# Performance work log

Hardware: AMD Instinct MI355X
Metric: run time of the kernel (lower is better)

## Reference

```python
import jax, jax.numpy as jnp
import numpy as np

N_EMBD = 1024
N_HEAD = 16
HEAD_DIM = N_EMBD // N_HEAD


def setup_inputs() -> dict:
    key = jax.random.key(0)
    ks = jax.random.split(key, 9)
    B, S = 4, 2048
    s = 1.0 / np.sqrt(N_EMBD)
    return {
        "x": jax.random.normal(ks[0], (B, S, N_EMBD), dtype=jnp.float32),
        "attention_mask": jnp.ones((B, S), dtype=jnp.int32),
        "Wq": jax.random.normal(ks[1], (N_EMBD, N_EMBD), jnp.float32) * s,
        "bq": jnp.zeros((N_EMBD,), jnp.float32),
        "Wk": jax.random.normal(ks[2], (N_EMBD, N_EMBD), jnp.float32) * s,
        "bk": jnp.zeros((N_EMBD,), jnp.float32),
        "Wv": jax.random.normal(ks[3], (N_EMBD, N_EMBD), jnp.float32) * s,
        "bv": jnp.zeros((N_EMBD,), jnp.float32),
        "Wo": jax.random.normal(ks[4], (N_EMBD, N_EMBD), jnp.float32) * s,
        "bo": jnp.zeros((N_EMBD,), jnp.float32),
    }


def _split_heads(t):  # [B,S,E] -> [B,H,S,D]
    B, S, _ = t.shape
    return t.reshape(B, S, N_HEAD, HEAD_DIM).transpose(0, 2, 1, 3)


def reference(x, attention_mask, Wq, bq, Wk, bk, Wv, bv, Wo, bo):
    B, S, E = x.shape
    q = _split_heads(x @ Wq.T + bq)
    k = _split_heads(x @ Wk.T + bk)
    v = _split_heads(x @ Wv.T + bv)
    # scores: [B,H,S,S]
    scores = jnp.einsum('bhqd,bhkd->bhqk', q, k) / np.sqrt(HEAD_DIM).astype(np.float32)
    # additive mask: 0 where mask==1, -inf where mask==0, broadcast over heads/query
    mask = jnp.where(attention_mask[:, None, None, :] == 0, -jnp.inf, 0.0).astype(scores.dtype)
    scores = scores + mask
    probs = jax.nn.softmax(scores, axis=-1)  # dropout p=0 -> identity
    ctx = jnp.einsum('bhqk,bhkd->bhqd', probs, v)
    out = ctx.transpose(0, 2, 1, 3).reshape(B, S, E)
    return out @ Wo.T + bo
```

## Files before the change

### kernel.cpp

```cpp
#include <hip/hip_runtime.h>

typedef __bf16 bf16;
typedef __attribute__((ext_vector_type(2))) bf16 bf16x2;
typedef __attribute__((ext_vector_type(4))) bf16 bf16x4;
typedef __attribute__((ext_vector_type(8))) bf16 bf16x8;
typedef __attribute__((ext_vector_type(4))) float f32x4;
typedef __attribute__((ext_vector_type(16))) float f32x16;
typedef __attribute__((ext_vector_type(4))) int i32x4;
typedef __attribute__((ext_vector_type(2))) int i32x2;

#define MFMA_BF16(a, b, c) __builtin_amdgcn_mfma_f32_16x16x32_bf16((a), (b), (c), 0, 0, 0)
#define MFMA32(a, b, c)    __builtin_amdgcn_mfma_f32_32x32x16_bf16((a), (b), (c), 0, 0, 0)

constexpr int S_LEN = 2048;
constexpr int EMB   = 1024;
constexpr int NHEAD = 16;
constexpr int HDIM  = 64;
constexpr int BATCH = 4;
constexpr int NTOK  = BATCH * S_LEN;

__device__ __forceinline__ void gload_lds16(const bf16* g, bf16* l) {
    __builtin_amdgcn_global_load_lds(
        (const __attribute__((address_space(1))) void*)g,
        (__attribute__((address_space(3))) void*)l, 16, 0, 0);
}

__device__ __forceinline__ int pkbf(float a, float b) {
    bf16x2 t; t[0] = (bf16)a; t[1] = (bf16)b;
    return __builtin_bit_cast(int, t);
}

#if __has_builtin(__builtin_amdgcn_permlane32_swap)
__device__ __forceinline__ i32x2 permswap(int a, int b) {
    return __builtin_amdgcn_permlane32_swap(a, b, false, false);
}
#else
__device__ __forceinline__ i32x2 permswap(int a, int b) {
    int as = __shfl_xor(a, 32);
    int bs = __shfl_xor(b, 32);
    int hx_ = (threadIdx.x >> 5) & 1;
    i32x2 r;
    r[0] = hx_ ? bs : a;
    r[1] = hx_ ? b : as;
    return r;
}
#endif

__global__ __launch_bounds__(256)
void cvt_f32_bf16(const float* __restrict__ src, bf16* __restrict__ dst, int n4) {
    int i = blockIdx.x * 256 + threadIdx.x;
    if (i < n4) {
        f32x4 v = ((const f32x4*)src)[i];
        bf16x4 o;
        o[0] = (bf16)v[0]; o[1] = (bf16)v[1]; o[2] = (bf16)v[2]; o[3] = (bf16)v[3];
        ((bf16x4*)dst)[i] = o;
    }
}

__global__ __launch_bounds__(256)
void cvt_w4(const float* __restrict__ s0, const float* __restrict__ s1,
            const float* __restrict__ s2, const float* __restrict__ s3,
            bf16* __restrict__ dst) {
    const int a = blockIdx.y;
    const float* s = a == 0 ? s0 : (a == 1 ? s1 : (a == 2 ? s2 : s3));
    int i = blockIdx.x * 256 + threadIdx.x;
    f32x4 v = ((const f32x4*)s)[i];
    bf16x4 o;
    o[0] = (bf16)v[0]; o[1] = (bf16)v[1]; o[2] = (bf16)v[2]; o[3] = (bf16)v[3];
    ((bf16x4*)(dst + (size_t)a * EMB * EMB))[i] = o;
}

__global__ __launch_bounds__(512)
void gemm256(const bf16* __restrict__ A,
             const bf16* __restrict__ W0, const bf16* __restrict__ W1, const bf16* __restrict__ W2,
             const float* __restrict__ b0, const float* __restrict__ b1, const float* __restrict__ b2,
             void* __restrict__ d0, void* __restrict__ d1, void* __restrict__ d2,
             int fused, float q_scale)
{
    __shared__ bf16 lds_a[2][2][128 * 32];
    __shared__ bf16 lds_b[2][2][256 * 32];

    const int fb  = blockIdx.x;
    const int xcd = fb & 7;
    const int loc = fb >> 3;
    const int xi  = xcd * 8 + (loc & 7);
    const int y   = loc >> 3;

    int seg, mode, n0;
    if (fused) { seg = y >> 2; n0 = (y & 3) * 256; mode = (seg == 2) ? 1 : 0; }
    else       { seg = 0;      n0 = y * 256;        mode = 2; }
    const bf16*  W    = seg == 0 ? W0 : (seg == 1 ? W1 : W2);
    const float* bias = seg == 0 ? b0 : (seg == 1 ? b1 : b2);
    void*        C    = seg == 0 ? d0 : (seg == 1 ? d1 : d2);
    const float  osc  = (fused && seg == 0) ? q_scale : 1.0f;

    const int tid  = threadIdx.x;
    const int lane = tid & 63;
    const int w    = tid >> 6;
    const int wr   = w >> 2;
    const int wc   = w & 3;
    const int quad = lane >> 4;
    const int l16  = lane & 15;
    const int m0   = xi * 128;

#define STAGE_A(BUF, H, T) {                                                        \
    int m_ = tid >> 2, s_ = tid & 3;                                                \
    gload_lds16(A + (size_t)(m0 + m_) * EMB + (T) * 64 + (H) * 32                   \
                  + ((s_ ^ ((m_ >> 1) & 3)) << 3),                                  \
                &lds_a[BUF][H][tid * 8]);                                           \
}
#define STAGE_B(BUF, H, T) {                                                        \
    _Pragma("unroll") for (int c_ = 0; c_ < 2; ++c_) {                              \
        int idx_ = c_ * 512 + tid;                                                  \
        int n_ = idx_ >> 2, s_ = idx_ & 3;                                          \
        gload_lds16(W + (size_t)(n0 + n_) * EMB + (T) * 64 + (H) * 32               \
                      + ((s_ ^ ((n_ >> 1) & 3)) << 3),                              \
                    &lds_b[BUF][H][idx_ * 8]);                                      \
    } }

#define READ_A(DST, BUF, H, G) {                                                    \
    _Pragma("unroll") for (int i_ = 0; i_ < 2; ++i_) {                              \
        int m_ = wr * 64 + (G) * 32 + i_ * 16 + l16;                                \
        DST[i_] = *(const bf16x8*)&lds_a[BUF][H][m_ * 32 + ((quad ^ ((m_ >> 1) & 3)) << 3)]; \
    } }
#define READ_B(DST, BUF, H) {                                                       \
    _Pragma("unroll") for (int j_ = 0; j_ < 4; ++j_) {                              \
        int n_ = wc * 64 + j_ * 16 + l16;                                           \
        DST[j_] = *(const bf16x8*)&lds_b[BUF][H][n_ * 32 + ((quad ^ ((n_ >> 1) & 3)) << 3)]; \
    } }

#define MFMA_PH(AF, BF, G) {                                                        \
    __builtin_amdgcn_s_setprio(1);                                                  \
    _Pragma("unroll") for (int i_ = 0; i_ < 2; ++i_)                                \
        _Pragma("unroll") for (int j_ = 0; j_ < 4; ++j_)                            \
            acc[(G) * 2 + i_][j_] = MFMA_BF16(AF[i_], BF[j_], acc[(G) * 2 + i_][j_]); \
    __builtin_amdgcn_s_setprio(0);                                                  \
}

    f32x4 acc[4][4] = {};

    STAGE_A(0, 0, 0) STAGE_B(0, 0, 0) STAGE_A(0, 1, 0) STAGE_B(0, 1, 0)
    asm volatile("s_waitcnt vmcnt(3)" ::: "memory");
    __builtin_amdgcn_s_barrier();
    __builtin_amdgcn_sched_barrier(0);

    for (int t = 0; t < 16; ++t) {
        const int cur  = t & 1;
        const int nxt  = cur ^ 1;
        const bool more = (t + 1 < 16);
        bf16x8 afr[2], bfr[4];

        READ_B(bfr, cur, 0)
        READ_A(afr, cur, 0, 0)
        if (more) STAGE_A(nxt, 0, t + 1)
        MFMA_PH(afr, bfr, 0)

        READ_A(afr, cur, 0, 1)
        if (more) STAGE_B(nxt, 0, t + 1)
        MFMA_PH(afr, bfr, 1)
        if (more) asm volatile("s_waitcnt vmcnt(3)" ::: "memory");
        else      asm volatile("s_waitcnt vmcnt(0)" ::: "memory");
        __builtin_amdgcn_s_barrier();
        __builtin_amdgcn_sched_barrier(0);

        READ_B(bfr, cur, 1)
        READ_A(afr, cur, 1, 0)
        if (more) STAGE_A(nxt, 1, t + 1)
        MFMA_PH(afr, bfr, 0)

        READ_A(afr, cur, 1, 1)
        if (more) STAGE_B(nxt, 1, t + 1)
        MFMA_PH(afr, bfr, 1)
        if (more) {
            asm volatile("s_waitcnt vmcnt(3)" ::: "memory");
            __builtin_amdgcn_s_barrier();
            __builtin_amdgcn_sched_barrier(0);
        }
    }

#undef STAGE_A
#undef STAGE_B
#undef READ_A
#undef READ_B
#undef MFMA_PH

    #pragma unroll
    for (int ii = 0; ii < 4; ++ii) {
        #pragma unroll
        for (int j = 0; j < 4; ++j) {
            int col = n0 + wc * 64 + j * 16 + l16;
            float bv = bias[col];
            int row0 = m0 + wr * 64 + ii * 16 + quad * 4;
            if (mode == 1) {
                int bb = row0 >> 11, s0 = row0 & 2047;
                int hh = col >> 6,   d  = col & 63;
                bf16x4 pk;
                #pragma unroll
                for (int r = 0; r < 4; ++r) pk[r] = (bf16)(acc[ii][j][r] + bv);
                *(bf16x4*)((bf16*)C + (size_t)((bb * NHEAD + hh) * HDIM + d) * S_LEN + s0) = pk;
            } else if (mode == 0) {
                #pragma unroll
                for (int r = 0; r < 4; ++r)
                    ((bf16*)C)[(size_t)(row0 + r) * EMB + col] = (bf16)((acc[ii][j][r] + bv) * osc);
            } else {
                #pragma unroll
                for (int r = 0; r < 4; ++r)
                    ((float*)C)[(size_t)(row0 + r) * EMB + col] = acc[ii][j][r] + bv;
            }
        }
    }
}

__global__ __launch_bounds__(512)
void flash_attn(const bf16* __restrict__ qg, const bf16* __restrict__ kg,
                const bf16* __restrict__ vtg, const int* __restrict__ maskg,
                bf16* __restrict__ ctx)
{
    __shared__ bf16  klds[2][64 * 64];
    __shared__ bf16  vlds[2][64 * 64];
    __shared__ bf16  bias_lds[2048];
    __shared__ float stat_lds[8][32];

    const int fb  = blockIdx.x;
    const int xcd = fb & 7;
    const int rr  = fb >> 3;
    const int qi  = rr & 7;
    const int gg  = rr >> 3;
    const int g   = gg * 8 + xcd;
    const int h   = g & 15;
    const int b   = g >> 4;
    const int q0  = qi * 256;

    const int tid  = threadIdx.x;
    const int lane = tid & 63;
    const int w    = tid >> 6;
    const int l32  = lane & 31;
    const int hx   = lane >> 5;

    const int srow  = tid >> 3;
    const int sslot = (tid & 7) ^ (srow & 7);

    int ok;
    {
        int i = tid * 4;
        i32x4 mv = *(const i32x4*)(maskg + b * S_LEN + i);
        bf16x4 bb;
        ok = 1;
        #pragma unroll
        for (int r = 0; r < 4; ++r) {
            ok &= (mv[r] != 0);
            bb[r] = mv[r] ? (bf16)0.f : (bf16)(-3.0e38f);
        }
        *(bf16x4*)&bias_lds[i] = bb;
    }
    const int allvalid = __syncthreads_and(ok);

    bf16x8 qf[4];
    {
        const bf16* qrow = qg + (size_t)(b * S_LEN + q0 + w * 32 + l32) * EMB + h * HDIM + hx * 8;
        qf[0] = *(const bf16x8*)(qrow);
        qf[1] = *(const bf16x8*)(qrow + 16);
        qf[2] = *(const bf16x8*)(qrow + 32);
        qf[3] = *(const bf16x8*)(qrow + 48);
    }

    const bf16* kgb = kg  + (size_t)b * S_LEN * EMB + h * HDIM;
    const bf16* vgb = vtg + (size_t)((b * NHEAD + h) * HDIM) * S_LEN;

    float mrow = -1e30f, lpart = 0.f;
    f32x16 o0, o1;
    #pragma unroll
    for (int r = 0; r < 16; ++r) { o0[r] = 0.f; o1[r] = 0.f; }

#define STAGE(BUF, KT) {                                                            \
    gload_lds16(kgb + (size_t)((KT) * 64 + srow) * EMB + sslot * 8,                 \
                &klds[BUF][tid * 8]);                                               \
    gload_lds16(vgb + (size_t)srow * S_LEN + (KT) * 64 + sslot * 8,                 \
                &vlds[BUF][tid * 8]);                                               \
}

#define LDSK(CUR, ROW, SB) (*(const bf16x8*)((const char*)&klds[CUR][0] + ((ROW) << 7) + ((((SB) ^ ((ROW) & 7))) << 4)))
#define LDSV(CUR, ROW, SB) (*(const bf16x8*)((const char*)&vlds[CUR][0] + ((ROW) << 7) + ((((SB) ^ ((ROW) & 7))) << 4)))

#define SUBTILE(CUR, KT, KK) {                                                      \
    f32x16 s_;                                                                      \
    _Pragma("unroll") for (int r_ = 0; r_ < 16; ++r_) s_[r_] = 0.f;                 \
    const int krow_ = (KK) * 32 + l32;                                              \
    __builtin_amdgcn_s_setprio(1);                                                  \
    s_ = MFMA32(LDSK(CUR, krow_, 0 * 2 + hx), qf[0], s_);                           \
    s_ = MFMA32(LDSK(CUR, krow_, 1 * 2 + hx), qf[1], s_);                           \
    s_ = MFMA32(LDSK(CUR, krow_, 2 * 2 + hx), qf[2], s_);                           \
    s_ = MFMA32(LDSK(CUR, krow_, 3 * 2 + hx), qf[3], s_);                           \
    __builtin_amdgcn_s_setprio(0);                                                  \
    if (!allvalid) {                                                                \
        _Pragma("unroll") for (int s4_ = 0; s4_ < 4; ++s4_) {                       \
            bf16x4 b4_ = *(const bf16x4*)&bias_lds[(KT) * 64 + (KK) * 32 + s4_ * 8 + hx * 4]; \
            _Pragma("unroll") for (int t_ = 0; t_ < 4; ++t_)                        \
                s_[4 * s4_ + t_] += (float)b4_[t_];                                 \
        }                                                                           \
    }                                                                               \
    float rmax_ = s_[0];                                                            \
    _Pragma("unroll") for (int r_ = 1; r_ < 16; ++r_) rmax_ = fmaxf(rmax_, s_[r_]); \
    rmax_ = fmaxf(rmax_, __shfl_xor(rmax_, 32));                                    \
    if (!__all(rmax_ <= mrow + 8.f)) {                                              \
        float mnew_  = fmaxf(mrow, rmax_);                                          \
        float alpha_ = __builtin_amdgcn_exp2f(mrow - mnew_);                        \
        mrow = mnew_; lpart *= alpha_;                                              \
        if (hx == 0) stat_lds[w][l32] = alpha_;                                     \
        _Pragma("unroll") for (int s4_ = 0; s4_ < 4; ++s4_) {                       \
            f32x4 a4_ = *(const f32x4*)&stat_lds[w][s4_ * 8 + hx * 4];              \
            _Pragma("unroll") for (int t_ = 0; t_ < 4; ++t_) {                      \
                o0[4 * s4_ + t_] *= a4_[t_]; o1[4 * s4_ + t_] *= a4_[t_];           \
            }                                                                       \
        }                                                                           \
    }                                                                               \
    bf16x8 pa0, pa1;                                                                \
    {                                                                               \
        float p_[8];                                                                \
        _Pragma("unroll") for (int r_ = 0; r_ < 8; ++r_) {                          \
            p_[r_] = __builtin_amdgcn_exp2f(s_[r_] - mrow); lpart += p_[r_];        \
        }                                                                           \
        i32x2 r0_ = permswap(pkbf(p_[0], p_[1]), pkbf(p_[4], p_[5]));               \
        i32x2 r1_ = permswap(pkbf(p_[2], p_[3]), pkbf(p_[6], p_[7]));               \
        i32x4 fw_; fw_[0] = r0_[0]; fw_[1] = r1_[0]; fw_[2] = r0_[1]; fw_[3] = r1_[1]; \
        pa0 = __builtin_bit_cast(bf16x8, fw_);                                      \
    }                                                                               \
    {                                                                               \
        float p_[8];                                                                \
        _Pragma("unroll") for (int r_ = 0; r_ < 8; ++r_) {                          \
            p_[r_] = __builtin_amdgcn_exp2f(s_[8 + r_] - mrow); lpart += p_[r_];    \
        }                                                                           \
        i32x2 r0_ = permswap(pkbf(p_[0], p_[1]), pkbf(p_[4], p_[5]));               \
        i32x2 r1_ = permswap(pkbf(p_[2], p_[3]), pkbf(p_[6], p_[7]));               \
        i32x4 fw_; fw_[0] = r0_[0]; fw_[1] = r1_[0]; fw_[2] = r0_[1]; fw_[3] = r1_[1]; \
        pa1 = __builtin_bit_cast(bf16x8, fw_);                                      \
    }                                                                               \
    __builtin_amdgcn_s_setprio(1);                                                  \
    o0 = MFMA32(pa0, LDSV(CUR, 0 * 32 + l32, (KK) * 4 + 0 * 2 + hx), o0);           \
    o1 = MFMA32(pa0, LDSV(CUR, 1 * 32 + l32, (KK) * 4 + 0 * 2 + hx), o1);           \
    o0 = MFMA32(pa1, LDSV(CUR, 0 * 32 + l32, (KK) * 4 + 1 * 2 + hx), o0);           \
    o1 = MFMA32(pa1, LDSV(CUR, 1 * 32 + l32, (KK) * 4 + 1 * 2 + hx), o1);           \
    __builtin_amdgcn_s_setprio(0);                                                  \
}

    STAGE(0, 0)
    __syncthreads();

    for (int kt = 0; kt < 32; ++kt) {
        const int cur = kt & 1;
        if (kt + 1 < 32) STAGE(cur ^ 1, kt + 1)
        SUBTILE(cur, kt, 0)
        SUBTILE(cur, kt, 1)
        __syncthreads();
    }

#undef SUBTILE
#undef LDSK
#undef LDSV
#undef STAGE

    float lrow = lpart + __shfl_xor(lpart, 32);
    float inv  = lrow > 0.f ? 1.f / lrow : 0.f;
    if (hx == 0) stat_lds[w][l32] = inv;
    #pragma unroll
    for (int s4 = 0; s4 < 4; ++s4) {
        f32x4 i4 = *(const f32x4*)&stat_lds[w][s4 * 8 + hx * 4];
        #pragma unroll
        for (int t = 0; t < 4; ++t) {
            size_t row = (size_t)(b * S_LEN + q0 + w * 32 + s4 * 8 + hx * 4 + t);
            bf16* cp = ctx + row * EMB + h * HDIM + l32;
            cp[0]  = (bf16)(o0[4 * s4 + t] * i4[t]);
            cp[32] = (bf16)(o1[4 * s4 + t] * i4[t]);
        }
    }
}

extern "C" void kernel_launch(void* const* d_in, const int* in_sizes, int n_in,
                              void* d_out, int out_size, void* d_ws, size_t ws_size,
                              hipStream_t stream)
{
    const float* x   = (const float*)d_in[0];
    const int*  mask = (const int*)d_in[1];
    const float* Wq  = (const float*)d_in[2];
    const float* bq  = (const float*)d_in[3];
    const float* Wk  = (const float*)d_in[4];
    const float* bk  = (const float*)d_in[5];
    const float* Wv  = (const float*)d_in[6];
    const float* bv  = (const float*)d_in[7];
    const float* Wo  = (const float*)d_in[8];
    const float* bo  = (const float*)d_in[9];
    (void)in_sizes; (void)n_in; (void)out_size; (void)ws_size;

    const size_t me = (size_t)NTOK * EMB;
    const size_t we = (size_t)EMB * EMB;
    bf16* xb  = (bf16*)d_ws;
    bf16* qb  = xb  + me;
    bf16* kb  = qb  + me;
    bf16* vt  = kb  + me;
    bf16* wqb = vt  + me;
    bf16* wkb = wqb + we;
    bf16* wvb = wkb + we;
    bf16* wob = wvb + we;
    bf16* cx  = xb;

    cvt_f32_bf16<<<(int)(me / 4 / 256), 256, 0, stream>>>(x, xb, (int)(me / 4));
    cvt_w4<<<dim3((int)(we / 4 / 256), 4), 256, 0, stream>>>(Wq, Wk, Wv, Wo, wqb);

    gemm256<<<dim3(64 * 12), 512, 0, stream>>>(
        xb, wqb, wkb, wvb, bq, bk, bv, qb, kb, vt, 1, 0.18033688011112042f);

    flash_attn<<<dim3(512), 512, 0, stream>>>(qb, kb, vt, mask, cx);

    gemm256<<<dim3(64 * 4), 512, 0, stream>>>(
        cx, wob, wob, wob, bo, bo, bo, d_out, d_out, d_out, 0, 1.0f);
}
```

Before: 297.7 us.

## Enlarge GEMM tile to 256x256 with triple-buffered K=32 pipeline

The projection GEMM block tile grows from 128x256 to 256x256, so each wave computes 128x64 with 32 accumulators instead of 16. This raises arithmetic intensity per global load. The K-loop now uses 32-wide steps with a three-stage LDS ring buffer, prefetching two steps ahead and needing one barrier per step instead of two. The costs are half as many blocks (384 and 128, so the output GEMM underfills the 256 CUs), more register pressure, and larger LDS use.

```diff
diff --git a/kernel.cpp b/kernel.cpp
--- a/kernel.cpp
+++ b/kernel.cpp
@@ -77,14 +77,14 @@
              void* __restrict__ d0, void* __restrict__ d1, void* __restrict__ d2,
              int fused, float q_scale)
 {
-    __shared__ bf16 lds_a[2][2][128 * 32];
-    __shared__ bf16 lds_b[2][2][256 * 32];
+    __shared__ bf16 la[3][256 * 32];
+    __shared__ bf16 lb[3][256 * 32];
 
     const int fb  = blockIdx.x;
     const int xcd = fb & 7;
     const int loc = fb >> 3;
-    const int xi  = xcd * 8 + (loc & 7);
-    const int y   = loc >> 3;
+    const int xi  = xcd * 4 + (loc & 3);
+    const int y   = loc >> 2;
 
     int seg, mode, n0;
     if (fused) { seg = y >> 2; n0 = (y & 3) * 256; mode = (seg == 2) ? 1 : 0; }
@@ -101,96 +101,66 @@
     const int wc   = w & 3;
     const int quad = lane >> 4;
     const int l16  = lane & 15;
-    const int m0   = xi * 128;
-
-#define STAGE_A(BUF, H, T) {                                                        \
-    int m_ = tid >> 2, s_ = tid & 3;                                                \
-    gload_lds16(A + (size_t)(m0 + m_) * EMB + (T) * 64 + (H) * 32                   \
-                  + ((s_ ^ ((m_ >> 1) & 3)) << 3),                                  \
-                &lds_a[BUF][H][tid * 8]);                                           \
-}
-#define STAGE_B(BUF, H, T) {                                                        \
+    const int m0   = xi * 256;
+
+#define STAGE_T(BI, T) {                                                            \
     _Pragma("unroll") for (int c_ = 0; c_ < 2; ++c_) {                              \
         int idx_ = c_ * 512 + tid;                                                  \
-        int n_ = idx_ >> 2, s_ = idx_ & 3;                                          \
-        gload_lds16(W + (size_t)(n0 + n_) * EMB + (T) * 64 + (H) * 32               \
-                      + ((s_ ^ ((n_ >> 1) & 3)) << 3),                              \
-                    &lds_b[BUF][H][idx_ * 8]);                                      \
+        int r_ = idx_ >> 2, s_ = idx_ & 3;                                          \
+        int co_ = (T) * 32 + ((s_ ^ ((r_ >> 1) & 3)) << 3);                         \
+        gload_lds16(A + (size_t)(m0 + r_) * EMB + co_, &la[BI][idx_ * 8]);          \
+        gload_lds16(W + (size_t)(n0 + r_) * EMB + co_, &lb[BI][idx_ * 8]);          \
     } }
 
-#define READ_A(DST, BUF, H, G) {                                                    \
-    _Pragma("unroll") for (int i_ = 0; i_ < 2; ++i_) {                              \
-        int m_ = wr * 64 + (G) * 32 + i_ * 16 + l16;                                \
-        DST[i_] = *(const bf16x8*)&lds_a[BUF][H][m_ * 32 + ((quad ^ ((m_ >> 1) & 3)) << 3)]; \
-    } }
-#define READ_B(DST, BUF, H) {                                                       \
-    _Pragma("unroll") for (int j_ = 0; j_ < 4; ++j_) {                              \
-        int n_ = wc * 64 + j_ * 16 + l16;                                           \
-        DST[j_] = *(const bf16x8*)&lds_b[BUF][H][n_ * 32 + ((quad ^ ((n_ >> 1) & 3)) << 3)]; \
-    } }
-
-#define MFMA_PH(AF, BF, G) {                                                        \
-    __builtin_amdgcn_s_setprio(1);                                                  \
-    _Pragma("unroll") for (int i_ = 0; i_ < 2; ++i_)                                \
-        _Pragma("unroll") for (int j_ = 0; j_ < 4; ++j_)                            \
-            acc[(G) * 2 + i_][j_] = MFMA_BF16(AF[i_], BF[j_], acc[(G) * 2 + i_][j_]); \
-    __builtin_amdgcn_s_setprio(0);                                                  \
-}
-
-    f32x4 acc[4][4] = {};
-
-    STAGE_A(0, 0, 0) STAGE_B(0, 0, 0) STAGE_A(0, 1, 0) STAGE_B(0, 1, 0)
-    asm volatile("s_waitcnt vmcnt(3)" ::: "memory");
+    f32x4 acc[8][4] = {};
+
+    STAGE_T(0, 0)
+    STAGE_T(1, 1)
+    asm volatile("s_waitcnt vmcnt(4)" ::: "memory");
     __builtin_amdgcn_s_barrier();
     __builtin_amdgcn_sched_barrier(0);
 
-    for (int t = 0; t < 16; ++t) {
-        const int cur  = t & 1;
-        const int nxt  = cur ^ 1;
-        const bool more = (t + 1 < 16);
-        bf16x8 afr[2], bfr[4];
-
-        READ_B(bfr, cur, 0)
-        READ_A(afr, cur, 0, 0)
-        if (more) STAGE_A(nxt, 0, t + 1)
-        MFMA_PH(afr, bfr, 0)
-
-        READ_A(afr, cur, 0, 1)
-        if (more) STAGE_B(nxt, 0, t + 1)
-        MFMA_PH(afr, bfr, 1)
-        if (more) asm volatile("s_waitcnt vmcnt(3)" ::: "memory");
-        else      asm volatile("s_waitcnt vmcnt(0)" ::: "memory");
-        __builtin_amdgcn_s_barrier();
-        __builtin_amdgcn_sched_barrier(0);
-
-        READ_B(bfr, cur, 1)
-        READ_A(afr, cur, 1, 0)
-        if (more) STAGE_A(nxt, 1, t + 1)
-        MFMA_PH(afr, bfr, 0)
-
-        READ_A(afr, cur, 1, 1)
-        if (more) STAGE_B(nxt, 1, t + 1)
-        MFMA_PH(afr, bfr, 1)
-        if (more) {
-            asm volatile("s_waitcnt vmcnt(3)" ::: "memory");
+    int cur = 0;
+    for (int t = 0; t < 32; ++t) {
+        int sb = cur + 2; if (sb >= 3) sb -= 3;
+        if (t + 2 < 32) STAGE_T(sb, t + 2)
+
+        bf16x8 afr[8], bfr[4];
+        #pragma unroll
+        for (int i = 0; i < 8; ++i) {
+            int m_ = wr * 128 + i * 16 + l16;
+            afr[i] = *(const bf16x8*)&la[cur][m_ * 32 + ((quad ^ ((m_ >> 1) & 3)) << 3)];
+        }
+        #pragma unroll
+        for (int j = 0; j < 4; ++j) {
+            int n_ = wc * 64 + j * 16 + l16;
+            bfr[j] = *(const bf16x8*)&lb[cur][n_ * 32 + ((quad ^ ((n_ >> 1) & 3)) << 3)];
+        }
+        __builtin_amdgcn_s_setprio(1);
+        #pragma unroll
+        for (int i = 0; i < 8; ++i)
+            #pragma unroll
+            for (int j = 0; j < 4; ++j)
+                acc[i][j] = MFMA_BF16(afr[i], bfr[j], acc[i][j]);
+        __builtin_amdgcn_s_setprio(0);
+
+        if (t + 2 < 32)      asm volatile("s_waitcnt vmcnt(4)" ::: "memory");
+        else if (t + 1 < 32) asm volatile("s_waitcnt vmcnt(0)" ::: "memory");
+        if (t + 1 < 32) {
             __builtin_amdgcn_s_barrier();
             __builtin_amdgcn_sched_barrier(0);
         }
-    }
-
-#undef STAGE_A
-#undef STAGE_B
-#undef READ_A
-#undef READ_B
-#undef MFMA_PH
+        cur = (cur + 1 == 3) ? 0 : cur + 1;
+    }
+#undef STAGE_T
 
     #pragma unroll
-    for (int ii = 0; ii < 4; ++ii) {
+    for (int ii = 0; ii < 8; ++ii) {
         #pragma unroll
         for (int j = 0; j < 4; ++j) {
             int col = n0 + wc * 64 + j * 16 + l16;
             float bv = bias[col];
-            int row0 = m0 + wr * 64 + ii * 16 + quad * 4;
+            int row0 = m0 + wr * 128 + ii * 16 + quad * 4;
             if (mode == 1) {
                 int bb = row0 >> 11, s0 = row0 & 2047;
                 int hh = col >> 6,   d  = col & 63;
@@ -406,11 +376,11 @@
     cvt_f32_bf16<<<(int)(me / 4 / 256), 256, 0, stream>>>(x, xb, (int)(me / 4));
     cvt_w4<<<dim3((int)(we / 4 / 256), 4), 256, 0, stream>>>(Wq, Wk, Wv, Wo, wqb);
 
-    gemm256<<<dim3(64 * 12), 512, 0, stream>>>(
+    gemm256<<<dim3(8 * 48), 512, 0, stream>>>(
         xb, wqb, wkb, wvb, bq, bk, bv, qb, kb, vt, 1, 0.18033688011112042f);
 
     flash_attn<<<dim3(512), 512, 0, stream>>>(qb, kb, vt, mask, cx);
 
-    gemm256<<<dim3(64 * 4), 512, 0, stream>>>(
+    gemm256<<<dim3(8 * 16), 512, 0, stream>>>(
         cx, wob, wob, wob, bo, bo, bo, d_out, d_out, d_out, 0, 1.0f);
 }
```

New measurement: 319.3 us. 1.07x slower.
